# Kernel tuning notes

Hardware: AMD Instinct MI355X
Metric: run time of the kernel (lower is better)

## Reference

```python
import jax, jax.numpy as jnp
import numpy as np

B, S, H = 2, 2048, 4096
NH, NKV, HD = 32, 8, 128
ROPE_THETA = 10000.0


def setup_inputs() -> dict:
    key = jax.random.key(0)
    ks = jax.random.split(key, 5)
    hidden_states = jax.random.normal(ks[0], (B, S, H), dtype=jnp.float32)
    position_ids = jnp.tile(jnp.arange(S, dtype=jnp.int64)[None, :], (B, 1))
    Wq = jax.random.normal(ks[1], (H, NH * HD), dtype=jnp.float32) * 0.02
    Wk = jax.random.normal(ks[2], (H, NKV * HD), dtype=jnp.float32) * 0.02
    Wv = jax.random.normal(ks[3], (H, NKV * HD), dtype=jnp.float32) * 0.02
    Wo = jax.random.normal(ks[4], (NH * HD, H), dtype=jnp.float32) * 0.02
    return {"hidden_states": hidden_states, "position_ids": position_ids,
            "Wq": Wq, "Wk": Wk, "Wv": Wv, "Wo": Wo}


def _rotate_half(x):
    d = x.shape[-1] // 2
    return jnp.concatenate([-x[..., d:], x[..., :d]], axis=-1)


def reference(hidden_states, position_ids, Wq, Wk, Wv, Wo):
    b, s, _ = hidden_states.shape
    # QKV projections (no bias)
    q = (hidden_states @ Wq).reshape(b, s, NH, HD).transpose(0, 2, 1, 3)   # [b,nh,s,hd]
    k = (hidden_states @ Wk).reshape(b, s, NKV, HD).transpose(0, 2, 1, 3)  # [b,nkv,s,hd]
    v = (hidden_states @ Wv).reshape(b, s, NKV, HD).transpose(0, 2, 1, 3)
    # RoPE: cos/sin from cached table == analytic computation at position_ids
    inv_freq = 1.0 / (ROPE_THETA ** (jnp.arange(0, HD, 2, dtype=jnp.float32) / HD))
    freqs = position_ids.astype(jnp.float32)[:, :, None] * inv_freq  # [b,s,hd/2]
    emb = jnp.concatenate([freqs, freqs], axis=-1)                   # [b,s,hd]
    cos = jnp.cos(emb)[:, None, :, :]  # unsqueeze_dim=1 -> [b,1,s,hd]
    sin = jnp.sin(emb)[:, None, :, :]
    q = q * cos + _rotate_half(q) * sin
    k = k * cos + _rotate_half(k) * sin
    # GQA: repeat kv heads to match query heads
    groups = NH // NKV
    k = jnp.repeat(k, groups, axis=1)
    v = jnp.repeat(v, groups, axis=1)
    # causal SDPA
    scale = 1.0 / jnp.sqrt(jnp.float32(HD))
    scores = jnp.einsum('bhqd,bhkd->bhqk', q, k) * scale
    causal = jnp.tril(jnp.ones((s, s), dtype=bool))
    scores = jnp.where(causal[None, None], scores, jnp.finfo(scores.dtype).min)
    attn = jax.nn.softmax(scores, axis=-1)
    out = jnp.einsum('bhqk,bhkd->bhqd', attn, v)
    out = out.transpose(0, 2, 1, 3).reshape(b, s, NH * HD)
    return out @ Wo
```

## Files before the change

kernel.cpp:

```cpp
#include <hip/hip_runtime.h>
#include <cstdint>
#include <cstddef>

typedef unsigned short u16;
typedef unsigned int u32;
typedef short short8 __attribute__((ext_vector_type(8)));
typedef float f32x4 __attribute__((ext_vector_type(4)));

__device__ __forceinline__ u16 f2bf(float f) {
  unsigned u = __float_as_uint(f);
  u += 0x7fffu + ((u >> 16) & 1u);
  return (u16)(u >> 16);
}
__device__ __forceinline__ float bf2f(u16 h) {
  return __uint_as_float(((unsigned)h) << 16);
}
__device__ __forceinline__ u32 pack_bf2(float lo, float hi) {
  return ((u32)f2bf(hi) << 16) | (u32)f2bf(lo);
}

typedef const __attribute__((address_space(1))) unsigned int gu32_t;
typedef __attribute__((address_space(3))) unsigned int su32_t;
__device__ __forceinline__ void gl2lds16(const void* g, void* l) {
  __builtin_amdgcn_global_load_lds((gu32_t*)g, (su32_t*)l, 16, 0, 0);
}

__device__ __forceinline__ f32x4 mfma_bf16(short8 a, short8 b, f32x4 c) {
  return __builtin_amdgcn_mfma_f32_16x16x32_bf16(a, b, c, 0, 0, 0);
}

__global__ __launch_bounds__(256) void f32_to_bf16_kernel(
    const float* __restrict__ x, u16* __restrict__ y, int n) {
  int i = (blockIdx.x * 256 + threadIdx.x) * 4;
  if (i + 3 < n) {
    float4 v = *(const float4*)(x + i);
    ushort4 o;
    o.x = f2bf(v.x); o.y = f2bf(v.y); o.z = f2bf(v.z); o.w = f2bf(v.w);
    *(ushort4*)(y + i) = o;
  }
}

__global__ __launch_bounds__(256) void transpose_w_kernel(
    const float* __restrict__ W, u16* __restrict__ Wt, int K, int N) {
  __shared__ float tile[32][33];
  int n0 = blockIdx.x * 32, k0 = blockIdx.y * 32;
  int tx = threadIdx.x, ty = threadIdx.y;
#pragma unroll
  for (int j = 0; j < 4; ++j)
    tile[ty + j * 8][tx] = W[(size_t)(k0 + ty + j * 8) * N + n0 + tx];
  __syncthreads();
#pragma unroll
  for (int j = 0; j < 4; ++j)
    Wt[(size_t)(n0 + ty + j * 8) * K + k0 + tx] = f2bf(tile[tx][ty + j * 8]);
}

__device__ __forceinline__ void tile_compute(const u16* __restrict__ as,
                                             const u16* __restrict__ bs,
                                             f32x4 (&acc)[8][4],
                                             int arow, int brow, int qoff) {
  short8 bfr[4], afr[4];
#pragma unroll
  for (int n = 0; n < 4; ++n)
    bfr[n] = *(const short8*)&bs[(brow + n * 16) * 32 + qoff];
#pragma unroll
  for (int m = 0; m < 4; ++m)
    afr[m] = *(const short8*)&as[(arow + m * 16) * 32 + qoff];
  __builtin_amdgcn_s_setprio(1);
#pragma unroll
  for (int m = 0; m < 4; ++m)
#pragma unroll
    for (int n = 0; n < 4; ++n)
      acc[m][n] = mfma_bf16(afr[m], bfr[n], acc[m][n]);
  __builtin_amdgcn_s_setprio(0);
#pragma unroll
  for (int m = 0; m < 4; ++m)
    afr[m] = *(const short8*)&as[(arow + (4 + m) * 16) * 32 + qoff];
  __builtin_amdgcn_s_setprio(1);
#pragma unroll
  for (int m = 0; m < 4; ++m)
#pragma unroll
    for (int n = 0; n < 4; ++n)
      acc[4 + m][n] = mfma_bf16(afr[m], bfr[n], acc[4 + m][n]);
  __builtin_amdgcn_s_setprio(0);
}

#define STAGE256(slot_, ko_)                                     \
  do {                                                           \
    u16* as_ = &lds4[slot_][0][0];                               \
    u16* bs_ = &lds4[slot_][1][0];                               \
    gl2lds16(ap + (ko_), as_ + w * 512);                         \
    gl2lds16(ap + (size_t)128 * K + (ko_), as_ + 4096 + w * 512);\
    gl2lds16(bp + (ko_), bs_ + w * 512);                         \
    gl2lds16(bp + (size_t)128 * K + (ko_), bs_ + 4096 + w * 512);\
  } while (0)

#define SBAR()                          \
  do {                                  \
    asm volatile("" ::: "memory");      \
    __builtin_amdgcn_s_barrier();       \
    asm volatile("" ::: "memory");      \
  } while (0)

template <bool BF16OUT>
__global__ __launch_bounds__(512, 2) void gemm_bt_256(
    const u16* __restrict__ A, const u16* __restrict__ Bt,
    float* __restrict__ Cf, u16* __restrict__ Cb, int K, int ldc) {
  __shared__ alignas(16) u16 lds4[4][2][8192];
  const int tid = threadIdx.x;
  const int w = tid >> 6, lane = tid & 63;
  const int lq = lane & 15, qd = lane >> 4;
  const int wm = w >> 2, wn = w & 3;
  const int m0 = blockIdx.y * 256, n0 = blockIdx.x * 256;
  const int r4 = lane >> 2;
  const int csw = ((lane & 3) ^ ((lane >> 3) & 3)) * 8;
  const int qoff = (qd ^ ((lq >> 1) & 3)) * 8;
  const int arow = wm * 128 + lq, brow = wn * 64 + lq;

  f32x4 acc[8][4] = {};
  const u16* ap = A + ((size_t)(m0 + w * 16 + r4) * K + csw);
  const u16* bp = Bt + ((size_t)(n0 + w * 16 + r4) * K + csw);
  const int nt = K >> 5;

  STAGE256(0, 0);
  STAGE256(1, 32);
  STAGE256(2, 64);

  for (int t = 0; t + 3 < nt; ++t) {
    STAGE256((t + 3) & 3, (t + 3) * 32);
    asm volatile("s_waitcnt vmcnt(12)" ::: "memory");
    SBAR();
    tile_compute(&lds4[t & 3][0][0], &lds4[t & 3][1][0], acc, arow, brow, qoff);
    SBAR();
  }
  asm volatile("s_waitcnt vmcnt(8)" ::: "memory");
  SBAR();
  tile_compute(&lds4[(nt - 3) & 3][0][0], &lds4[(nt - 3) & 3][1][0], acc, arow, brow, qoff);
  asm volatile("s_waitcnt vmcnt(4)" ::: "memory");
  SBAR();
  tile_compute(&lds4[(nt - 2) & 3][0][0], &lds4[(nt - 2) & 3][1][0], acc, arow, brow, qoff);
  asm volatile("s_waitcnt vmcnt(0)" ::: "memory");
  SBAR();
  tile_compute(&lds4[(nt - 1) & 3][0][0], &lds4[(nt - 1) & 3][1][0], acc, arow, brow, qoff);

#pragma unroll
  for (int m = 0; m < 8; ++m) {
    const int row = m0 + wm * 128 + m * 16 + qd * 4;
#pragma unroll
    for (int n = 0; n < 4; ++n) {
      const int col = n0 + wn * 64 + n * 16 + lq;
#pragma unroll
      for (int r = 0; r < 4; ++r) {
        if (BF16OUT)
          Cb[(size_t)(row + r) * ldc + col] = f2bf(acc[m][n][r]);
        else
          Cf[(size_t)(row + r) * ldc + col] = acc[m][n][r];
      }
    }
  }
}

#undef STAGE256

__global__ __launch_bounds__(256) void rope_kernel(
    const u16* __restrict__ src, u16* __restrict__ dst,
    const int* __restrict__ pos_ids, int nh, int src_col0, int dst_ld, int total,
    float scale) {
  int idx = blockIdx.x * 256 + threadIdx.x;
  if (idx >= total) return;
  int i = idx & 63;
  int t = idx >> 6;
  int hh = t % nh;
  int m = t / nh;
  float pos = (float)pos_ids[m];
  float inv = exp2f(-(float)i * 0.20762050593046016f);
  float f = pos * inv;
  float c = cosf(f) * scale, s = sinf(f) * scale;
  const u16* sp = src + (size_t)m * 6144 + src_col0 + hh * 128;
  float x0 = bf2f(sp[i]);
  float x1 = bf2f(sp[i + 64]);
  u16* dp = dst + (size_t)m * dst_ld + hh * 128;
  dp[i] = f2bf(x0 * c - x1 * s);
  dp[i + 64] = f2bf(x1 * c + x0 * s);
}

__global__ __launch_bounds__(256) void vt_kernel(
    const u16* __restrict__ src, u16* __restrict__ vt) {
  __shared__ u16 tile[32][33];
  int s0 = blockIdx.x * 32;
  int d0 = blockIdx.y * 32;
  int bz = blockIdx.z;
  int b = bz >> 3, kvh = bz & 7;
  int tx = threadIdx.x, ty = threadIdx.y;
#pragma unroll
  for (int j = 0; j < 4; ++j)
    tile[ty + j * 8][tx] =
        src[(size_t)(b * 2048 + s0 + ty + j * 8) * 6144 + 5120 + kvh * 128 + d0 + tx];
  __syncthreads();
#pragma unroll
  for (int j = 0; j < 4; ++j)
    vt[((size_t)(b * 8 + kvh) * 128 + d0 + ty + j * 8) * 2048 + s0 + tx] =
        tile[tx][ty + j * 8];
}

#define PS_LD 76

__device__ __forceinline__ void load_q_frag(short8 (&qf)[2][4], const u16* __restrict__ Q,
                                            int b, int q0, int w, int lq, int qd, int h) {
  const u16* qp = Q + ((size_t)(b * 2048 + q0 + w * 32 + lq) * 4096 + h * 128 + qd * 8);
#pragma unroll
  for (int n = 0; n < 2; ++n)
#pragma unroll
    for (int ks = 0; ks < 4; ++ks)
      qf[n][ks] = *(const short8*)(qp + (size_t)n * 16 * 4096 + ks * 32);
}

__device__ __forceinline__ void store_o(u16* __restrict__ O, const f32x4 (&ot)[2][8],
                                        const float* lsum, int b, int q0,
                                        int w, int lq, int qd, int h) {
#pragma unroll
  for (int n = 0; n < 2; ++n) {
    const float inv = 1.f / lsum[n];
    const size_t row = (size_t)(b * 2048 + q0 + w * 32 + n * 16 + lq);
    u16* op = O + row * 4096 + h * 128 + qd * 4;
#pragma unroll
    for (int mt = 0; mt < 8; ++mt) {
      u32 a = pack_bf2(ot[n][mt][0] * inv, ot[n][mt][1] * inv);
      u32 c = pack_bf2(ot[n][mt][2] * inv, ot[n][mt][3] * inv);
      *(uint2*)(op + mt * 16) = make_uint2(a, c);
    }
  }
}

__global__ __launch_bounds__(256, 2) void flash_kernel(
    const u16* __restrict__ Q, const u16* __restrict__ K,
    const u16* __restrict__ Vt, u16* __restrict__ O) {
  __shared__ alignas(16) u16 Ks[64 * 128];
  __shared__ alignas(16) u16 Vs[128 * 64];
  __shared__ alignas(16) u16 Ps[4][32 * PS_LD];

  const int tid = threadIdx.x;
  const int w = tid >> 6, lane = tid & 63;
  const int lq = lane & 15, qd = lane >> 4;
  const int lq7 = lq & 7;
  const int bh = blockIdx.y;
  const int b = bh >> 5, h = bh & 31, kvh = h >> 2;
  const int p = blockIdx.x;
  const int nhi = 32 - 2 * p;
  const int nlo = 2 * p + 2;
  const int nsteps = nhi + nlo;

  const int rk = lane >> 4, pk = lane & 15;
  const int ckA = (pk ^ rk) * 8, ckB = (pk ^ (4 + rk)) * 8;
  const int rv = lane >> 3;
  const int cv = ((lane & 7) ^ rv) * 8;

  const u16* ksrc = K + ((size_t)(b * 2048 + w * 16 + rk) * 1024) + kvh * 128;
  const u16* vsrc = Vt + ((size_t)((b * 8 + kvh) * 128 + w * 32 + rv) * 2048) + cv;
  u16* kdst = &Ks[(w * 16) * 128] + lane * 8;
  u16* vdst = &Vs[(w * 32) * 64] + lane * 8;

  int q0 = (15 - p) * 128;
  short8 qf[2][4];
  load_q_frag(qf, Q, b, q0, w, lq, qd, h);

  f32x4 ot[2][8] = {};
  float mprev[2] = {-1e30f, -1e30f}, lsum[2] = {0.f, 0.f};

  uint4 kreg[4], vreg[4];
  kreg[0] = *(const uint4*)(ksrc + ckA);
  kreg[1] = *(const uint4*)(ksrc + 4096 + ckB);
  kreg[2] = *(const uint4*)(ksrc + 8192 + ckA);
  kreg[3] = *(const uint4*)(ksrc + 12288 + ckB);
  vreg[0] = *(const uint4*)(vsrc);
  vreg[1] = *(const uint4*)(vsrc + 8 * 2048);
  vreg[2] = *(const uint4*)(vsrc + 16 * 2048);
  vreg[3] = *(const uint4*)(vsrc + 24 * 2048);
  *(uint4*)(kdst) = kreg[0];
  *(uint4*)(kdst + 512) = kreg[1];
  *(uint4*)(kdst + 1024) = kreg[2];
  *(uint4*)(kdst + 1536) = kreg[3];
  *(uint4*)(vdst) = vreg[0];
  *(uint4*)(vdst + 512) = vreg[1];
  *(uint4*)(vdst + 1024) = vreg[2];
  *(uint4*)(vdst + 1536) = vreg[3];
  asm volatile("s_waitcnt lgkmcnt(0)" ::: "memory");
  __builtin_amdgcn_s_barrier();

  for (int s = 0; s < nsteps; ++s) {
    const int kv0 = (s < nhi ? s : s - nhi) * 64;

    if (s + 1 < nsteps) {
      const int sn = s + 1;
      const int kv0n = (sn < nhi ? sn : sn - nhi) * 64;
      const u16* kp_ = ksrc + (size_t)kv0n * 1024;
      kreg[0] = *(const uint4*)(kp_ + ckA);
      kreg[1] = *(const uint4*)(kp_ + 4096 + ckB);
      kreg[2] = *(const uint4*)(kp_ + 8192 + ckA);
      kreg[3] = *(const uint4*)(kp_ + 12288 + ckB);
      const u16* vp_ = vsrc + kv0n;
      vreg[0] = *(const uint4*)(vp_);
      vreg[1] = *(const uint4*)(vp_ + 8 * 2048);
      vreg[2] = *(const uint4*)(vp_ + 16 * 2048);
      vreg[3] = *(const uint4*)(vp_ + 24 * 2048);
    }

    f32x4 st[4][2] = {};
#pragma unroll
    for (int ks = 0; ks < 4; ++ks) {
      short8 kf[4];
#pragma unroll
      for (int m = 0; m < 4; ++m)
        kf[m] = *(const short8*)&Ks[(m * 16 + lq) * 128 + ((ks * 4 + qd) ^ lq7) * 8];
      __builtin_amdgcn_s_setprio(1);
#pragma unroll
      for (int m = 0; m < 4; ++m)
#pragma unroll
        for (int n = 0; n < 2; ++n)
          st[m][n] = mfma_bf16(kf[m], qf[n][ks], st[m][n]);
      __builtin_amdgcn_s_setprio(0);
    }

    if (kv0 + 63 > q0) {
#pragma unroll
      for (int n = 0; n < 2; ++n) {
        const int qrow = q0 + w * 32 + n * 16 + lq;
#pragma unroll
        for (int m = 0; m < 4; ++m) {
          const int kvb = kv0 + m * 16 + qd * 4;
#pragma unroll
          for (int r = 0; r < 4; ++r)
            if (kvb + r > qrow) st[m][n][r] = -1e30f;
        }
      }
    }

#pragma unroll
    for (int n = 0; n < 2; ++n) {
      float t = st[0][n][0];
#pragma unroll
      for (int m = 0; m < 4; ++m)
#pragma unroll
        for (int r = 0; r < 4; ++r) t = fmaxf(t, st[m][n][r]);
      t = fmaxf(t, __shfl_xor(t, 16));
      t = fmaxf(t, __shfl_xor(t, 32));
      const float mnew = fmaxf(mprev[n], t);
      const float alpha = __expf(mprev[n] - mnew);
      mprev[n] = mnew;

      float rs = 0.f;
      u32 pk2[4][2];
#pragma unroll
      for (int m = 0; m < 4; ++m) {
        float p0 = __expf(st[m][n][0] - mnew);
        float p1 = __expf(st[m][n][1] - mnew);
        float p2 = __expf(st[m][n][2] - mnew);
        float p3 = __expf(st[m][n][3] - mnew);
        rs += (p0 + p1) + (p2 + p3);
        pk2[m][0] = pack_bf2(p0, p1);
        pk2[m][1] = pack_bf2(p2, p3);
      }
      rs += __shfl_xor(rs, 16);
      rs += __shfl_xor(rs, 32);
      lsum[n] = lsum[n] * alpha + rs;

      u16* pw = &Ps[w][(n * 16 + lq) * PS_LD + qd * 4];
#pragma unroll
      for (int m = 0; m < 4; ++m)
        *(uint2*)(pw + m * 16) = make_uint2(pk2[m][0], pk2[m][1]);

#pragma unroll
      for (int mt = 0; mt < 8; ++mt)
#pragma unroll
        for (int r = 0; r < 4; ++r) ot[n][mt][r] *= alpha;
    }

#pragma unroll
    for (int kst = 0; kst < 2; ++kst) {
      short8 bp[2];
#pragma unroll
      for (int n = 0; n < 2; ++n)
        bp[n] = *(const short8*)&Ps[w][(n * 16 + lq) * PS_LD + kst * 32 + qd * 8];
#pragma unroll
      for (int mt = 0; mt < 8; ++mt) {
        short8 av = *(const short8*)&Vs[(mt * 16 + lq) * 64 + ((kst * 4 + qd) ^ lq7) * 8];
        __builtin_amdgcn_s_setprio(1);
#pragma unroll
        for (int n = 0; n < 2; ++n)
          ot[n][mt] = mfma_bf16(av, bp[n], ot[n][mt]);
        __builtin_amdgcn_s_setprio(0);
      }
    }

    asm volatile("s_waitcnt lgkmcnt(0)" ::: "memory");
    __builtin_amdgcn_s_barrier();

    if (s + 1 < nsteps) {
      *(uint4*)(kdst) = kreg[0];
      *(uint4*)(kdst + 512) = kreg[1];
      *(uint4*)(kdst + 1024) = kreg[2];
      *(uint4*)(kdst + 1536) = kreg[3];
      *(uint4*)(vdst) = vreg[0];
      *(uint4*)(vdst + 512) = vreg[1];
      *(uint4*)(vdst + 1024) = vreg[2];
      *(uint4*)(vdst + 1536) = vreg[3];
      asm volatile("s_waitcnt lgkmcnt(0)" ::: "memory");
      __builtin_amdgcn_s_barrier();
    }

    if (s == nhi - 1) {
      store_o(O, ot, lsum, b, q0, w, lq, qd, h);
      q0 = p * 128;
      load_q_frag(qf, Q, b, q0, w, lq, qd, h);
#pragma unroll
      for (int n = 0; n < 2; ++n) {
        mprev[n] = -1e30f;
        lsum[n] = 0.f;
#pragma unroll
        for (int mt = 0; mt < 8; ++mt)
#pragma unroll
          for (int r = 0; r < 4; ++r) ot[n][mt][r] = 0.f;
      }
    }
  }

  store_o(O, ot, lsum, b, q0, w, lq, qd, h);
}

extern "C" void kernel_launch(void* const* d_in, const int* in_sizes, int n_in,
                              void* d_out, int out_size, void* d_ws, size_t ws_size,
                              hipStream_t stream) {
  const float* hidden = (const float*)d_in[0];
  const int* pos = (const int*)d_in[1];
  const float* Wq = (const float*)d_in[2];
  const float* Wk = (const float*)d_in[3];
  const float* Wv = (const float*)d_in[4];
  const float* Wo = (const float*)d_in[5];
  float* out = (float*)d_out;

  char* ws = (char*)d_ws;
  u16* hbf   = (u16*)(ws);
  u16* wqkvt = (u16*)(ws + 33554432ull);
  u16* wot   = (u16*)(ws + 83886080ull);
  u16* qkvbf = (u16*)(ws + 117440512ull);
  u16* qbf   = (u16*)(ws + 167772160ull);
  u16* kbf   = (u16*)(ws + 201326592ull);
  u16* vt    = (u16*)(ws + 209715200ull);
  u16* obf   = (u16*)(ws + 218103808ull);

  f32_to_bf16_kernel<<<16384, 256, 0, stream>>>(hidden, hbf, 16777216);
  transpose_w_kernel<<<dim3(128, 128), dim3(32, 8), 0, stream>>>(Wq, wqkvt, 4096, 4096);
  transpose_w_kernel<<<dim3(32, 128), dim3(32, 8), 0, stream>>>(Wk, wqkvt + (size_t)4096 * 4096, 4096, 1024);
  transpose_w_kernel<<<dim3(32, 128), dim3(32, 8), 0, stream>>>(Wv, wqkvt + (size_t)5120 * 4096, 4096, 1024);
  transpose_w_kernel<<<dim3(128, 128), dim3(32, 8), 0, stream>>>(Wo, wot, 4096, 4096);

  gemm_bt_256<true><<<dim3(24, 16), 512, 0, stream>>>(hbf, wqkvt, nullptr, qkvbf, 4096, 6144);

  rope_kernel<<<32768, 256, 0, stream>>>(qkvbf, qbf, pos, 32, 0, 4096, 8388608, 0.08838834764831845f);
  rope_kernel<<<8192, 256, 0, stream>>>(qkvbf, kbf, pos, 8, 4096, 1024, 2097152, 1.0f);

  vt_kernel<<<dim3(64, 4, 16), dim3(32, 8), 0, stream>>>(qkvbf, vt);

  flash_kernel<<<dim3(8, 64), 256, 0, stream>>>(qbf, kbf, vt, obf);

  gemm_bt_256<false><<<dim3(16, 16), 512, 0, stream>>>(obf, wot, out, nullptr, 4096, 4096);
}
```

Baseline: 868.5 us.

## Restructure GEMM main loop into 8-phase ping-pong pipeline with K=64 tiles

Replaces the 4-slot, K=32 GEMM pipeline with a double-buffered K=64 LDS layout (two 64KB halves) and an 8-phase schedule. Each phase interleaves LDS fragment reads, a quarter of the next tile's global-to-LDS loads, and a 4x2 block of MFMAs, with sched_barriers and fine-grained vmcnt waits. The aim is to overlap global loads with matrix math and cut per-K-step barrier overhead. It adds a new XOR swizzle, more barriers per tile, and LDS use of 128KB per block, which may reduce occupancy below the declared two blocks per CU.

```diff
diff --git a/kernel.cpp b/kernel.cpp
--- a/kernel.cpp
+++ b/kernel.cpp
@@ -28,6 +28,13 @@
 __device__ __forceinline__ f32x4 mfma_bf16(short8 a, short8 b, f32x4 c) {
   return __builtin_amdgcn_mfma_f32_16x16x32_bf16(a, b, c, 0, 0, 0);
 }
+
+#define SBAR()                          \
+  do {                                  \
+    asm volatile("" ::: "memory");      \
+    __builtin_amdgcn_s_barrier();       \
+    asm volatile("" ::: "memory");      \
+  } while (0)
 
 __global__ __launch_bounds__(256) void f32_to_bf16_kernel(
     const float* __restrict__ x, u16* __restrict__ y, int n) {
@@ -54,93 +61,121 @@
     Wt[(size_t)(n0 + ty + j * 8) * K + k0 + tx] = f2bf(tile[tx][ty + j * 8]);
 }
 
-__device__ __forceinline__ void tile_compute(const u16* __restrict__ as,
-                                             const u16* __restrict__ bs,
-                                             f32x4 (&acc)[8][4],
-                                             int arow, int brow, int qoff) {
-  short8 bfr[4], afr[4];
-#pragma unroll
-  for (int n = 0; n < 4; ++n)
-    bfr[n] = *(const short8*)&bs[(brow + n * 16) * 32 + qoff];
-#pragma unroll
-  for (int m = 0; m < 4; ++m)
-    afr[m] = *(const short8*)&as[(arow + m * 16) * 32 + qoff];
-  __builtin_amdgcn_s_setprio(1);
-#pragma unroll
-  for (int m = 0; m < 4; ++m)
-#pragma unroll
-    for (int n = 0; n < 4; ++n)
-      acc[m][n] = mfma_bf16(afr[m], bfr[n], acc[m][n]);
-  __builtin_amdgcn_s_setprio(0);
-#pragma unroll
-  for (int m = 0; m < 4; ++m)
-    afr[m] = *(const short8*)&as[(arow + (4 + m) * 16) * 32 + qoff];
-  __builtin_amdgcn_s_setprio(1);
-#pragma unroll
-  for (int m = 0; m < 4; ++m)
-#pragma unroll
-    for (int n = 0; n < 4; ++n)
-      acc[4 + m][n] = mfma_bf16(afr[m], bfr[n], acc[4 + m][n]);
-  __builtin_amdgcn_s_setprio(0);
-}
-
-#define STAGE256(slot_, ko_)                                     \
-  do {                                                           \
-    u16* as_ = &lds4[slot_][0][0];                               \
-    u16* bs_ = &lds4[slot_][1][0];                               \
-    gl2lds16(ap + (ko_), as_ + w * 512);                         \
-    gl2lds16(ap + (size_t)128 * K + (ko_), as_ + 4096 + w * 512);\
-    gl2lds16(bp + (ko_), bs_ + w * 512);                         \
-    gl2lds16(bp + (size_t)128 * K + (ko_), bs_ + 4096 + w * 512);\
-  } while (0)
-
-#define SBAR()                          \
-  do {                                  \
-    asm volatile("" ::: "memory");      \
-    __builtin_amdgcn_s_barrier();       \
-    asm volatile("" ::: "memory");      \
-  } while (0)
-
 template <bool BF16OUT>
-__global__ __launch_bounds__(512, 2) void gemm_bt_256(
+__global__ __launch_bounds__(512, 2) void gemm_bt_8p(
     const u16* __restrict__ A, const u16* __restrict__ Bt,
     float* __restrict__ Cf, u16* __restrict__ Cb, int K, int ldc) {
-  __shared__ alignas(16) u16 lds4[4][2][8192];
+  __shared__ alignas(16) u16 lds[65536];
   const int tid = threadIdx.x;
   const int w = tid >> 6, lane = tid & 63;
   const int lq = lane & 15, qd = lane >> 4;
+  const int lq7 = lq & 7;
   const int wm = w >> 2, wn = w & 3;
   const int m0 = blockIdx.y * 256, n0 = blockIdx.x * 256;
-  const int r4 = lane >> 2;
-  const int csw = ((lane & 3) ^ ((lane >> 3) & 3)) * 8;
-  const int qoff = (qd ^ ((lq >> 1) & 3)) * 8;
-  const int arow = wm * 128 + lq, brow = wn * 64 + lq;
+
+  const int srow = lane >> 3;
+  const int schk = (lane & 7) ^ srow;
+  const int arow_base = (w & 3) * 16 + (w >> 2) * 128;
+  const int brow_base = (w >> 1) * 64 + (w & 1) * 16;
+  const u16* aS = A + (size_t)(m0 + arow_base + srow) * K + schk * 8;
+  const u16* bS = Bt + (size_t)(n0 + brow_base + srow) * K + schk * 8;
+  const int dA = arow_base * 64;
+  const int dB = 16384 + brow_base * 64;
+
+  const int a_rd = (wm * 128 + lq) * 64;
+  const int b_rd = 16384 + (wn * 64 + lq) * 64;
+  const int cs0 = (qd ^ lq7) * 8;
+  const int cs1 = ((4 + qd) ^ lq7) * 8;
 
   f32x4 acc[8][4] = {};
-  const u16* ap = A + ((size_t)(m0 + w * 16 + r4) * K + csw);
-  const u16* bp = Bt + ((size_t)(n0 + w * 16 + r4) * K + csw);
-  const int nt = K >> 5;
-
-  STAGE256(0, 0);
-  STAGE256(1, 32);
-  STAGE256(2, 64);
-
-  for (int t = 0; t + 3 < nt; ++t) {
-    STAGE256((t + 3) & 3, (t + 3) * 32);
-    asm volatile("s_waitcnt vmcnt(12)" ::: "memory");
-    SBAR();
-    tile_compute(&lds4[t & 3][0][0], &lds4[t & 3][1][0], acc, arow, brow, qoff);
-    SBAR();
-  }
-  asm volatile("s_waitcnt vmcnt(8)" ::: "memory");
+  short8 a0[4][2], a1[4][2], b0[2][2], b1[2][2];
+
+#define SA(beta, r, j, kt)                                              \
+  gl2lds16(aS + (size_t)((r) * 64 + (j) * 8) * K + (size_t)(kt) * 64,   \
+           &lds[(beta) * 32768 + dA + (r) * 4096 + (j) * 512])
+#define SB(beta, r, j, kt)                                              \
+  gl2lds16(bS + (size_t)((r) * 32 + (j) * 8) * K + (size_t)(kt) * 64,   \
+           &lds[(beta) * 32768 + dB + (r) * 2048 + (j) * 512])
+#define SAR(beta, r, kt) do { SA(beta, r, 0, kt); SA(beta, r, 1, kt); } while (0)
+#define SBR(beta, r, kt) do { SB(beta, r, 0, kt); SB(beta, r, 1, kt); } while (0)
+
+#define RDA(arr, mb, beta)                                                        \
+  do {                                                                            \
+    _Pragma("unroll") for (int m = 0; m < 4; ++m) {                               \
+      arr[m][0] = *(const short8*)&lds[(beta) * 32768 + a_rd + ((mb) + m) * 1024 + cs0]; \
+      arr[m][1] = *(const short8*)&lds[(beta) * 32768 + a_rd + ((mb) + m) * 1024 + cs1]; \
+    }                                                                             \
+  } while (0)
+#define RDB(arr, nb, beta)                                                        \
+  do {                                                                            \
+    _Pragma("unroll") for (int n = 0; n < 2; ++n) {                               \
+      arr[n][0] = *(const short8*)&lds[(beta) * 32768 + b_rd + ((nb) + n) * 1024 + cs0]; \
+      arr[n][1] = *(const short8*)&lds[(beta) * 32768 + b_rd + ((nb) + n) * 1024 + cs1]; \
+    }                                                                             \
+  } while (0)
+#define MMQ(AF, BF, MB, NB)                                                       \
+  do {                                                                            \
+    _Pragma("unroll") for (int m = 0; m < 4; ++m)                                 \
+      _Pragma("unroll") for (int n = 0; n < 2; ++n) {                             \
+        acc[(MB) + m][(NB) + n] = mfma_bf16(AF[m][0], BF[n][0], acc[(MB) + m][(NB) + n]); \
+        acc[(MB) + m][(NB) + n] = mfma_bf16(AF[m][1], BF[n][1], acc[(MB) + m][(NB) + n]); \
+      }                                                                           \
+  } while (0)
+
+#define PH(BODY_RD, BODY_ST, BODY_MM, VN)                \
+  do {                                                   \
+    BODY_RD;                                             \
+    BODY_ST;                                             \
+    SBAR();                                              \
+    __builtin_amdgcn_sched_barrier(0);                   \
+    __builtin_amdgcn_s_setprio(1);                       \
+    BODY_MM;                                             \
+    __builtin_amdgcn_s_setprio(0);                       \
+    __builtin_amdgcn_sched_barrier(0);                   \
+    asm volatile("s_waitcnt vmcnt(" VN ")" ::: "memory");\
+    SBAR();                                              \
+  } while (0)
+
+  const int niter = K >> 7;
+
+  SAR(0, 0, 0); SBR(0, 0, 0);
+  SBR(0, 1, 0); SAR(0, 1, 0);
+  SAR(1, 0, 1); SBR(1, 0, 1);
+  SBR(1, 1, 1);
+  asm volatile("s_waitcnt vmcnt(10)" ::: "memory");
   SBAR();
-  tile_compute(&lds4[(nt - 3) & 3][0][0], &lds4[(nt - 3) & 3][1][0], acc, arow, brow, qoff);
-  asm volatile("s_waitcnt vmcnt(4)" ::: "memory");
-  SBAR();
-  tile_compute(&lds4[(nt - 2) & 3][0][0], &lds4[(nt - 2) & 3][1][0], acc, arow, brow, qoff);
-  asm volatile("s_waitcnt vmcnt(0)" ::: "memory");
-  SBAR();
-  tile_compute(&lds4[(nt - 1) & 3][0][0], &lds4[(nt - 1) & 3][1][0], acc, arow, brow, qoff);
+
+  for (int i = 0; i + 1 < niter; ++i) {
+    const int t1 = 2 * i + 1, t2 = 2 * i + 2, t3 = 2 * i + 3;
+    PH(RDA(a0, 0, 0); RDB(b0, 0, 0), SAR(1, 1, t1), MMQ(a0, b0, 0, 0), "6");
+    PH(RDB(b1, 2, 0),                SAR(0, 0, t2), MMQ(a0, b1, 0, 2), "6");
+    PH(RDA(a1, 4, 0),                SBR(0, 0, t2), MMQ(a1, b1, 4, 2), "6");
+    PH(,                             SBR(0, 1, t2), MMQ(a1, b0, 4, 0), "6");
+    PH(RDA(a0, 0, 1); RDB(b0, 0, 1), SAR(0, 1, t2), MMQ(a0, b0, 0, 0), "6");
+    PH(RDB(b1, 2, 1),                SAR(1, 0, t3), MMQ(a0, b1, 0, 2), "6");
+    PH(RDA(a1, 4, 1),                SBR(1, 0, t3), MMQ(a1, b1, 4, 2), "6");
+    PH(,                             SBR(1, 1, t3), MMQ(a1, b0, 4, 0), "6");
+  }
+  {
+    const int t1 = 2 * niter - 1;
+    PH(RDA(a0, 0, 0); RDB(b0, 0, 0), SAR(1, 1, t1), MMQ(a0, b0, 0, 0), "6");
+    PH(RDB(b1, 2, 0),              , MMQ(a0, b1, 0, 2), "6");
+    PH(RDA(a1, 4, 0),              , MMQ(a1, b1, 4, 2), "4");
+    PH(,                           , MMQ(a1, b0, 4, 0), "2");
+    PH(RDA(a0, 0, 1); RDB(b0, 0, 1),, MMQ(a0, b0, 0, 0), "0");
+    PH(RDB(b1, 2, 1),              , MMQ(a0, b1, 0, 2), "0");
+    PH(RDA(a1, 4, 1),              , MMQ(a1, b1, 4, 2), "0");
+    PH(,                           , MMQ(a1, b0, 4, 0), "0");
+  }
+
+#undef SA
+#undef SB
+#undef SAR
+#undef SBR
+#undef RDA
+#undef RDB
+#undef MMQ
+#undef PH
 
 #pragma unroll
   for (int m = 0; m < 8; ++m) {
@@ -158,8 +193,6 @@
     }
   }
 }
-
-#undef STAGE256
 
 __global__ __launch_bounds__(256) void rope_kernel(
     const u16* __restrict__ src, u16* __restrict__ dst,
@@ -453,7 +486,7 @@
   transpose_w_kernel<<<dim3(32, 128), dim3(32, 8), 0, stream>>>(Wv, wqkvt + (size_t)5120 * 4096, 4096, 1024);
   transpose_w_kernel<<<dim3(128, 128), dim3(32, 8), 0, stream>>>(Wo, wot, 4096, 4096);
 
-  gemm_bt_256<true><<<dim3(24, 16), 512, 0, stream>>>(hbf, wqkvt, nullptr, qkvbf, 4096, 6144);
+  gemm_bt_8p<true><<<dim3(24, 16), 512, 0, stream>>>(hbf, wqkvt, nullptr, qkvbf, 4096, 6144);
 
   rope_kernel<<<32768, 256, 0, stream>>>(qkvbf, qbf, pos, 32, 0, 4096, 8388608, 0.08838834764831845f);
   rope_kernel<<<8192, 256, 0, stream>>>(qkvbf, kbf, pos, 8, 4096, 1024, 2097152, 1.0f);
@@ -462,5 +495,5 @@
 
   flash_kernel<<<dim3(8, 64), 256, 0, stream>>>(qbf, kbf, vt, obf);
 
-  gemm_bt_256<false><<<dim3(16, 16), 512, 0, stream>>>(obf, wot, out, nullptr, 4096, 4096);
-}
+  gemm_bt_8p<false><<<dim3(16, 16), 512, 0, stream>>>(obf, wot, out, nullptr, 4096, 4096);
+}
```

After: 981.9 us. +13.1%, slower.
